# Kernel tuning notes

Hardware: AMD Instinct MI355X
Metric: run time of the kernel (lower is better)

Reference implementation:

```python
import jax, jax.numpy as jnp
import numpy as np

EPS = 1e-5
HEADS = 24
HEAD_DIM = 128


def _layernorm_noaffine(x):
    # LayerNorm over last dim (head_dim), elementwise_affine=False
    mu = jnp.mean(x, axis=-1, keepdims=True)
    var = jnp.mean(jnp.square(x - mu), axis=-1, keepdims=True)
    return (x - mu) / jnp.sqrt(var + EPS)


def _apply_rope(x, cos, sin):
    # diffusers apply_rotary_emb, use_real_unbind_dim=-2, sequence_dim=1
    # x: [B, S_img, H, D]; cos/sin: [S_img, D]
    x_real, x_imag = jnp.split(x, 2, axis=-1)               # halves of D
    x_rot = jnp.concatenate([-x_imag, x_real], axis=-1)
    return x * cos[None, :, None, :] + x_rot * sin[None, :, None, :]


def setup_inputs() -> dict:
    key = jax.random.key(0)
    ks = jax.random.split(key, 8)
    B, T, I, D = 2, 256, 1024, 3072
    inner = HEADS * HEAD_DIM
    return {
        "hidden_states": jax.random.normal(ks[0], (B, I, D), jnp.float32),
        "encoder_hidden_states": jax.random.normal(ks[1], (B, T, D), jnp.float32),
        "cos": jax.random.uniform(ks[2], (I, HEAD_DIM), jnp.float32),
        "sin": jax.random.uniform(ks[3], (I, HEAD_DIM), jnp.float32),
        "w_qkv": jax.random.normal(ks[4], (D, 3 * inner), jnp.float32) * 0.02,
        "b_qkv": jax.random.normal(ks[5], (3 * inner,), jnp.float32) * 0.02,
        "w_out": jax.random.normal(ks[6], (inner, D), jnp.float32) * 0.02,
        "b_out": jax.random.normal(ks[7], (D,), jnp.float32) * 0.02,
    }


def reference(hidden_states, encoder_hidden_states, cos, sin, w_qkv, b_qkv, w_out, b_out):
    text_len = encoder_hidden_states.shape[1]
    x = jnp.concatenate([encoder_hidden_states, hidden_states], axis=1)  # [B, S, D]
    B, S, _ = x.shape
    qkv = x @ w_qkv + b_qkv                                  # [B, S, 3*inner]
    q, k, v = jnp.split(qkv, 3, axis=-1)
    q = q.reshape(B, S, HEADS, HEAD_DIM)
    k = k.reshape(B, S, HEADS, HEAD_DIM)
    v = v.reshape(B, S, HEADS, HEAD_DIM)
    q = _layernorm_noaffine(q)
    k = _layernorm_noaffine(k)
    # partial RoPE: image tokens only
    q = jnp.concatenate([q[:, :text_len], _apply_rope(q[:, text_len:], cos, sin)], axis=1)
    k = jnp.concatenate([k[:, :text_len], _apply_rope(k[:, text_len:], cos, sin)], axis=1)
    # non-causal attention, scale = 1/sqrt(head_dim)
    scale = 1.0 / np.sqrt(HEAD_DIM).astype(np.float32)
    scores = jnp.einsum('bqhd,bkhd->bhqk', q, k) * scale
    attn = jax.nn.softmax(scores, axis=-1)
    out = jnp.einsum('bhqk,bkhd->bqhd', attn, v).reshape(B, S, HEADS * HEAD_DIM)
    out = out @ w_out + b_out                                # [B, S, D]
    return out[:, text_len:, :], out[:, :text_len, :]
```

## Files before the change

### kernel.cpp

```cpp
#include <hip/hip_runtime.h>

typedef unsigned short u16;
typedef __attribute__((ext_vector_type(8))) short bf16x8;
typedef __attribute__((ext_vector_type(4))) float f32x4;
typedef __attribute__((ext_vector_type(16))) float f32x16;

typedef const __attribute__((address_space(1))) void* gptr_t;
typedef __attribute__((address_space(3))) void* lptr_t;

__device__ __forceinline__ unsigned cvtpk_bf16(float a, float b){
  unsigned r; asm("v_cvt_pk_bf16_f32 %0, %1, %2" : "=v"(r) : "v"(a), "v"(b)); return r;
}
__device__ __forceinline__ u16 f2bf(float x){ return (u16)cvtpk_bf16(x, x); }
__device__ __forceinline__ float bf2f(u16 u){ union{unsigned i; float f;} v; v.i = ((unsigned)u)<<16; return v.f; }
__device__ __forceinline__ float fexp2(float x){ float r; asm("v_exp_f32 %0, %1" : "=v"(r) : "v"(x)); return r; }
__device__ __forceinline__ float vmax16(f32x16 v){
  float a0 = fmaxf(v[0],v[1]),  a1 = fmaxf(v[2],v[3]),  a2 = fmaxf(v[4],v[5]),  a3 = fmaxf(v[6],v[7]);
  float a4 = fmaxf(v[8],v[9]),  a5 = fmaxf(v[10],v[11]),a6 = fmaxf(v[12],v[13]),a7 = fmaxf(v[14],v[15]);
  float b0 = fmaxf(a0,a1), b1 = fmaxf(a2,a3), b2 = fmaxf(a4,a5), b3 = fmaxf(a6,a7);
  return fmaxf(fmaxf(b0,b1), fmaxf(b2,b3));
}

__global__ __launch_bounds__(256) void prep_x_kernel(const float* __restrict__ hs,
                                                     const float* __restrict__ ehs,
                                                     u16* __restrict__ A){
  int idx = blockIdx.x*256 + threadIdx.x;
  int v = idx*4;
  int m = v/3072, c = v - m*3072;
  int b = m/1280, s = m - b*1280;
  const float* src = (s < 256) ? (ehs + ((size_t)(b*256+s))*3072 + c)
                               : (hs  + ((size_t)(b*1024+(s-256)))*3072 + c);
  float4 f = *(const float4*)src;
  uint2 o; o.x = cvtpk_bf16(f.x, f.y); o.y = cvtpk_bf16(f.z, f.w);
  *(uint2*)(A + v) = o;
}

__global__ __launch_bounds__(256) void transpose_w_kernel(const float* __restrict__ W,
                                                          u16* __restrict__ Wt,
                                                          int K, int N){
  __shared__ float t[64][36];
  int k0 = blockIdx.y*64, n0 = blockIdx.x*32;
  int tid = threadIdx.x;
  #pragma unroll
  for (int i=0;i<2;i++){
    int cell = i*256 + tid; int kl = cell>>3, nc = cell&7;
    *(float4*)&t[kl][nc*4] = *(const float4*)&W[(size_t)(k0+kl)*N + n0 + nc*4];
  }
  __syncthreads();
  #pragma unroll
  for (int i=0;i<2;i++){
    int chunk = i*256 + tid; int nl = chunk>>4, kc = chunk&15;
    float a = t[kc*4+0][nl], b2 = t[kc*4+1][nl], c2 = t[kc*4+2][nl], d2 = t[kc*4+3][nl];
    uint2 u; u.x = cvtpk_bf16(a, b2); u.y = cvtpk_bf16(c2, d2);
    *(uint2*)&Wt[(size_t)(n0+nl)*K + k0 + kc*4] = u;
  }
}

__global__ __launch_bounds__(512) void gemm_qkv_kernel(const u16* __restrict__ A,
                                                       const u16* __restrict__ Bt,
                                                       const float* __restrict__ bias,
                                                       u16* __restrict__ C){
  const int K = 3072, N = 9216;
  __shared__ __align__(16) u16 lds[57344];
  int tid = threadIdx.x, wv = tid>>6, lane = tid&63;
  int wm = wv>>2, wn = wv&3;
  int l15 = lane&15, l4 = lane>>4;

  int bid = blockIdx.x;
  int wg = (bid&7)*60 + (bid>>3);
  int bm = wg/48, bn = wg%48;
  int m0 = bm*256, n0 = bn*192;

  int rlane = lane>>2;
  int schn = (lane&3) ^ ((lane>>3)&3);
  const u16* aS = A + (size_t)(m0 + wv*32 + rlane)*K + schn*8;
  int brow = n0 + wv*32 + rlane; if (brow > 9215) brow = 9215;
  const u16* bS = Bt + (size_t)brow*K + schn*8;

  auto stagePair = [&](int G){
    u16* base = lds + (G&3)*14336;
    size_t ko = (size_t)G*32;
    #pragma unroll
    for (int j=0;j<2;j++)
      __builtin_amdgcn_global_load_lds((gptr_t)(aS + (size_t)j*16*K + ko),
                                       (lptr_t)(base + (wv*2+j)*512), 16,0,0);
    if (wv < 6){
      #pragma unroll
      for (int j=0;j<2;j++)
        __builtin_amdgcn_global_load_lds((gptr_t)(bS + (size_t)j*16*K + ko),
                                         (lptr_t)(base + 8192 + (wv*2+j)*512), 16,0,0);
    }
  };

  int fcs = l4 ^ ((l15>>1)&3);
  f32x4 acc[8][3];
  #pragma unroll
  for (int r=0;r<8;r++)
    #pragma unroll
    for (int c=0;c<3;c++)
      #pragma unroll
      for (int q=0;q<4;q++) acc[r][c][q] = 0.f;

  stagePair(0); stagePair(1); stagePair(2);
  asm volatile("s_waitcnt vmcnt(4)" ::: "memory");
  __builtin_amdgcn_s_barrier();

  auto group = [&](int G, bool issue){
    const u16* rA = lds + (G&3)*14336;
    const u16* rB = rA + 8192;
    bf16x8 af[8], bfv[3];
    #pragma unroll
    for (int r=0;r<8;r++) af[r] = *(const bf16x8*)(rA + (wm*128 + r*16 + l15)*32 + fcs*8);
    #pragma unroll
    for (int c=0;c<3;c++) bfv[c] = *(const bf16x8*)(rB + (wn*48 + c*16 + l15)*32 + fcs*8);
    if (issue) stagePair(G+3);
    __builtin_amdgcn_s_setprio(1);
    #pragma unroll
    for (int r=0;r<8;r++)
      #pragma unroll
      for (int c=0;c<3;c++)
        acc[r][c] = __builtin_amdgcn_mfma_f32_16x16x32_bf16(af[r], bfv[c], acc[r][c], 0,0,0);
    __builtin_amdgcn_s_setprio(0);
  };

  for (int G=0; G<93; ++G){
    group(G, true);
    asm volatile("s_waitcnt vmcnt(4)" ::: "memory");
    __builtin_amdgcn_s_barrier();
  }
  group(93,false); asm volatile("s_waitcnt vmcnt(2)" ::: "memory"); __builtin_amdgcn_s_barrier();
  group(94,false); asm volatile("s_waitcnt vmcnt(0)" ::: "memory"); __builtin_amdgcn_s_barrier();
  group(95,false);

  #pragma unroll
  for (int r=0;r<8;r++){
    int row = m0 + wm*128 + r*16 + l4*4;
    #pragma unroll
    for (int c=0;c<3;c++){
      int col = n0 + wn*48 + c*16 + l15;
      float bv = bias[col];
      #pragma unroll
      for (int q=0;q<4;q++)
        C[(size_t)(row+q)*N + col] = f2bf(acc[r][c][q] + bv);
    }
  }
}

__global__ __launch_bounds__(256) void gemm_bt_kernel(const u16* __restrict__ A,
                                                      const u16* __restrict__ Bt,
                                                      const float* __restrict__ bias,
                                                      float* __restrict__ Cf,
                                                      int K, int N){
  __shared__ u16 As[2][4096];
  __shared__ u16 Bs[2][4096];
  int tid = threadIdx.x, wv = tid>>6, lane = tid&63;
  int l15 = lane & 15, l4 = lane >> 4;
  int m0 = blockIdx.y*128, n0 = blockIdx.x*128;
  int wr = wv>>1, wc = wv&1;

  f32x4 acc[4][4];
  #pragma unroll
  for (int i=0;i<4;i++)
    #pragma unroll
    for (int j=0;j<4;j++)
      #pragma unroll
      for (int r=0;r<4;r++) acc[i][j][r] = 0.f;

  const int NT = K >> 5;

  auto stage = [&](int buf, int kt){
    #pragma unroll
    for (int i=0;i<2;i++){
      int c = (wv*2+i)*64 + lane; int row = c>>2, kc = c&3;
      const u16* s = A + (size_t)(m0+row)*K + kt + kc*8;
      __builtin_amdgcn_global_load_lds((gptr_t)s, (lptr_t)(&As[buf][(wv*2+i)*512]), 16, 0, 0);
    }
    #pragma unroll
    for (int i=0;i<2;i++){
      int c = (wv*2+i)*64 + lane; int row = c>>2, kc = c&3;
      const u16* s = Bt + (size_t)(n0+row)*K + kt + kc*8;
      __builtin_amdgcn_global_load_lds((gptr_t)s, (lptr_t)(&Bs[buf][(wv*2+i)*512]), 16, 0, 0);
    }
  };

  stage(0, 0);
  __syncthreads();
  for (int t=0; t<NT; t++){
    int cur = t & 1;
    if (t+1 < NT) stage(cur^1, (t+1)*32);
    bf16x8 af[4], bfr[4];
    #pragma unroll
    for (int i=0;i<4;i++){
      af[i]  = *(const bf16x8*)&As[cur][(wr*64 + i*16 + l15)*32 + l4*8];
      bfr[i] = *(const bf16x8*)&Bs[cur][(wc*64 + i*16 + l15)*32 + l4*8];
    }
    #pragma unroll
    for (int i=0;i<4;i++)
      #pragma unroll
      for (int j=0;j<4;j++)
        acc[i][j] = __builtin_amdgcn_mfma_f32_16x16x32_bf16(af[i], bfr[j], acc[i][j], 0,0,0);
    __syncthreads();
  }

  #pragma unroll
  for (int i=0;i<4;i++){
    int row = m0 + wr*64 + i*16 + l4*4;
    #pragma unroll
    for (int j=0;j<4;j++){
      int col = n0 + wc*64 + j*16 + l15;
      float bv = bias[col];
      #pragma unroll
      for (int r=0;r<4;r++){
        int rr = row + r;
        int bb = rr / 1280; int s = rr - bb*1280;
        float* dst = (s < 256) ? (Cf + 6291456 + ((size_t)(bb*256 + s))*3072)
                               : (Cf + ((size_t)(bb*1024 + (s-256)))*3072);
        dst[col] = acc[i][j][r] + bv;
      }
    }
  }
}

__device__ __forceinline__ void ln_head(const u16* __restrict__ in, u16* __restrict__ out,
                                        const float* __restrict__ cosb, const float* __restrict__ sinb,
                                        int lane, int s, float scale){
  float x0 = bf2f(in[lane]), x1 = bf2f(in[64+lane]);
  float sum = x0 + x1;
  #pragma unroll
  for (int off=32; off>=1; off>>=1) sum += __shfl_xor(sum, off);
  float mean = sum * 0.0078125f;
  float d0 = x0-mean, d1 = x1-mean;
  float vs = d0*d0 + d1*d1;
  #pragma unroll
  for (int off=32; off>=1; off>>=1) vs += __shfl_xor(vs, off);
  float rstd = rsqrtf(vs*0.0078125f + 1e-5f);
  float y0 = d0*rstd, y1 = d1*rstd;
  if (s >= 256){
    int p = s - 256;
    float c0 = cosb[p*128 + lane], c1 = cosb[p*128 + 64 + lane];
    float s0 = sinb[p*128 + lane], s1 = sinb[p*128 + 64 + lane];
    float t0 = y0*c0 - y1*s0;
    float t1 = y1*c1 + y0*s1;
    y0 = t0; y1 = t1;
  }
  out[lane]    = f2bf(y0*scale);
  out[64+lane] = f2bf(y1*scale);
}

__global__ __launch_bounds__(256) void ln_rope_kernel(const u16* __restrict__ qkv,
                                                      const float* __restrict__ cosb,
                                                      const float* __restrict__ sinb,
                                                      u16* __restrict__ Q, u16* __restrict__ Kd){
  int g = blockIdx.x*4 + (threadIdx.x>>6);
  int lane = threadIdx.x & 63;
  int h = g % 24; int m = g / 24;
  int b = m / 1280; int s = m - b*1280;
  const u16* base = qkv + (size_t)m*9216 + h*128;
  size_t ho = ((size_t)(b*24 + h)*1280 + s)*128;
  ln_head(base,        Q  + ho, cosb, sinb, lane, s, 0.12751512f);
  ln_head(base + 3072, Kd + ho, cosb, sinb, lane, s, 1.0f);
}

__global__ __launch_bounds__(256) void v_transpose_kernel(const u16* __restrict__ qkv,
                                                          u16* __restrict__ Vt){
  __shared__ u16 tl[16384];
  int tid = threadIdx.x;
  int blk = blockIdx.x;
  int st = blk % 10; int bh = blk / 10; int b = bh/24, h = bh - b*24;
  #pragma unroll
  for (int i=0;i<8;i++){
    int idx = i*256 + tid; int s = idx>>4, dc = idx&15;
    int m = b*1280 + st*128 + s;
    bf16x8 v = *(const bf16x8*)(qkv + (size_t)m*9216 + 6144 + h*128 + dc*8);
    *(bf16x8*)(tl + (s*16 + (dc ^ ((s>>3)&7)))*8) = v;
  }
  __syncthreads();
  #pragma unroll
  for (int i=0;i<8;i++){
    int idx = i*256 + tid; int d = idx>>4, sc = idx&15;
    union { u16 t[8]; bf16x8 v; } tmp;
    #pragma unroll
    for (int j=0;j<8;j++){
      int s = sc*8 + j;
      tmp.t[j] = tl[(s*16 + ((d>>3) ^ ((s>>3)&7)))*8 + (d&7)];
    }
    *(bf16x8*)(Vt + ((size_t)bh*128 + d)*1280 + st*128 + sc*8) = tmp.v;
  }
}

__global__ __launch_bounds__(256) void attn_kernel(const u16* __restrict__ Q,
                                                   const u16* __restrict__ Kg,
                                                   const u16* __restrict__ Vt,
                                                   u16* __restrict__ AO){
  __shared__ __align__(16) u16 smem[32768];
  int tid = threadIdx.x, wv = tid>>6, lane = tid&63;
  int l31 = lane & 31, hi = lane >> 5;
  int blk = blockIdx.x;
  int qt = blk % 10; int bh = blk / 10;
  int b = bh / 24; int h = bh - b*24;
  const u16* Qb = Q  + (size_t)bh*1280*128;
  const u16* Kb = Kg + (size_t)bh*1280*128;
  const u16* Vb = Vt + (size_t)bh*128*1280;
  int q0 = qt*128 + wv*32;

  bf16x8 qf[8];
  #pragma unroll
  for (int ds=0; ds<8; ds++)
    qf[ds] = *(const bf16x8*)(Qb + (size_t)(q0 + l31)*128 + ds*16 + hi*8);

  f32x16 o[4];
  #pragma unroll
  for (int dc=0; dc<4; dc++)
    #pragma unroll
    for (int r=0;r<16;r++) o[dc][r] = 0.f;
  float mrun = -1e30f, lrun = 0.f;

  auto stage = [&](int t){
    int s0 = t*64; int bu = t&1;
    u16* Ksb = smem + bu*8192;
    u16* Vsb = smem + 16384 + bu*8192;
    #pragma unroll
    for (int i=0;i<4;i++){
      int c = (wv*4+i)*64 + lane; int key = c>>4, dc16 = c&15;
      const u16* src = Kb + (size_t)(s0+key)*128 + ((dc16 ^ (key&7))<<3);
      __builtin_amdgcn_global_load_lds((gptr_t)src, (lptr_t)(Ksb + (wv*4+i)*512), 16, 0, 0);
    }
    #pragma unroll
    for (int i=0;i<4;i++){
      int c = (wv*4+i)*64 + lane; int d = c>>3, kc = c&7;
      const u16* src = Vb + (size_t)d*1280 + s0 + ((kc ^ (d&7))<<3);
      __builtin_amdgcn_global_load_lds((gptr_t)src, (lptr_t)(Vsb + (wv*4+i)*512), 16, 0, 0);
    }
  };

  auto compute = [&](int t){
    const u16* Ks = smem + (t&1)*8192;
    const u16* Vs = smem + 16384 + (t&1)*8192;
    f32x16 sA, sB, sC, sD;
    #pragma unroll
    for (int r=0;r<16;r++){ sA[r]=0.f; sB[r]=0.f; sC[r]=0.f; sD[r]=0.f; }
    __builtin_amdgcn_s_setprio(1);
    #pragma unroll
    for (int dp=0; dp<4; dp++){
      int dsE = 2*dp, dsO = 2*dp+1;
      int chE = dsE*2 + hi, chO = dsO*2 + hi;
      bf16x8 k0E = *(const bf16x8*)(Ks + (l31*16      + (chE ^ (l31 & 7)))*8);
      bf16x8 k1E = *(const bf16x8*)(Ks + ((32+l31)*16 + (chE ^ (l31 & 7)))*8);
      bf16x8 k0O = *(const bf16x8*)(Ks + (l31*16      + (chO ^ (l31 & 7)))*8);
      bf16x8 k1O = *(const bf16x8*)(Ks + ((32+l31)*16 + (chO ^ (l31 & 7)))*8);
      sA = __builtin_amdgcn_mfma_f32_32x32x16_bf16(k0E, qf[dsE], sA, 0,0,0);
      sC = __builtin_amdgcn_mfma_f32_32x32x16_bf16(k1E, qf[dsE], sC, 0,0,0);
      sB = __builtin_amdgcn_mfma_f32_32x32x16_bf16(k0O, qf[dsO], sB, 0,0,0);
      sD = __builtin_amdgcn_mfma_f32_32x32x16_bf16(k1O, qf[dsO], sD, 0,0,0);
    }
    __builtin_amdgcn_s_setprio(0);
    f32x16 sacc0, sacc1;
    #pragma unroll
    for (int r=0;r<16;r++){ sacc0[r] = sA[r]+sB[r]; sacc1[r] = sC[r]+sD[r]; }

    float mt = fmaxf(vmax16(sacc0), vmax16(sacc1));
    mt = fmaxf(mt, __shfl_xor(mt, 32));
    int noresc = __all(mt <= mrun + 11.5f);
    float mnew, corr;
    if (noresc){ mnew = mrun; corr = 1.f; }
    else       { mnew = fmaxf(mrun, mt); corr = fexp2(mrun - mnew); }
    mrun = mnew;
    float p[32];
    float ps0=0.f, ps1=0.f, ps2=0.f, ps3=0.f;
    #pragma unroll
    for (int r=0;r<8;r++){ p[r]    = fexp2(sacc0[r]   - mnew); ps0 += p[r]; }
    #pragma unroll
    for (int r=0;r<8;r++){ p[8+r]  = fexp2(sacc0[8+r] - mnew); ps1 += p[8+r]; }
    #pragma unroll
    for (int r=0;r<8;r++){ p[16+r] = fexp2(sacc1[r]   - mnew); ps2 += p[16+r]; }
    #pragma unroll
    for (int r=0;r<8;r++){ p[24+r] = fexp2(sacc1[8+r] - mnew); ps3 += p[24+r]; }
    float ps = (ps0+ps1) + (ps2+ps3);
    ps += __shfl_xor(ps, 32);
    lrun = lrun*corr + ps;
    if (!noresc){
      #pragma unroll
      for (int dc=0; dc<4; dc++)
        #pragma unroll
        for (int r=0;r<16;r++) o[dc][r] *= corr;
    }

    bf16x8 pf[4];
    #pragma unroll
    for (int c=0;c<4;c++){
      const float* pp = p + (c>>1)*16 + (c&1)*8;
      unsigned x0 = cvtpk_bf16(pp[0], pp[1]);
      unsigned y0 = cvtpk_bf16(pp[4], pp[5]);
      unsigned x1 = cvtpk_bf16(pp[2], pp[3]);
      unsigned y1 = cvtpk_bf16(pp[6], pp[7]);
      asm volatile("v_permlane32_swap_b32 %0, %1" : "+v"(x0), "+v"(y0));
      asm volatile("v_permlane32_swap_b32 %0, %1" : "+v"(x1), "+v"(y1));
      union { unsigned u[4]; bf16x8 v; } wb;
      wb.u[0]=x0; wb.u[1]=x1; wb.u[2]=y0; wb.u[3]=y1;
      pf[c] = wb.v;
    }
    __builtin_amdgcn_s_setprio(1);
    #pragma unroll
    for (int c=0;c<4;c++){
      #pragma unroll
      for (int dc=0;dc<4;dc++){
        int d = dc*32 + l31;
        bf16x8 vf = *(const bf16x8*)(Vs + (d*8 + ((2*c+hi) ^ (d&7)))*8);
        o[dc] = __builtin_amdgcn_mfma_f32_32x32x16_bf16(vf, pf[c], o[dc], 0,0,0);
      }
    }
    __builtin_amdgcn_s_setprio(0);
  };

  stage(0); stage(1);
  for (int t=0; t<19; ++t){
    asm volatile("s_waitcnt vmcnt(8)" ::: "memory");
    __builtin_amdgcn_s_barrier();
    compute(t);
    __builtin_amdgcn_s_barrier();
    if (t <= 17) stage(t+2);
  }
  asm volatile("s_waitcnt vmcnt(0)" ::: "memory");
  __builtin_amdgcn_s_barrier();
  compute(19);

  float rl = 1.f / lrun;
  __syncthreads();
  u16* ob = smem + wv*4096;
  #pragma unroll
  for (int dc=0; dc<4; dc++){
    #pragma unroll
    for (int rp=0; rp<8; rp++){
      int d = dc*32 + 2*(rp&1) + 8*(rp>>1) + 4*hi;
      unsigned u = cvtpk_bf16(o[dc][2*rp]*rl, o[dc][2*rp+1]*rl);
      int chs = (d>>3) ^ (l31 & 7);
      *(unsigned*)(ob + l31*128 + chs*8 + (d&7)) = u;
    }
  }
  __syncthreads();
  #pragma unroll
  for (int i=0;i<8;i++){
    int idx = i*64 + lane; int q = idx>>4, c8 = idx&15;
    bf16x8 vv = *(const bf16x8*)(ob + q*128 + ((c8 ^ (q&7))<<3));
    *(bf16x8*)(AO + (size_t)(b*1280 + q0 + q)*3072 + h*128 + c8*8) = vv;
  }
}

extern "C" void kernel_launch(void* const* d_in, const int* in_sizes, int n_in,
                              void* d_out, int out_size, void* d_ws, size_t ws_size,
                              hipStream_t stream){
  (void)in_sizes; (void)n_in; (void)out_size; (void)ws_size;
  const float* hs   = (const float*)d_in[0];
  const float* ehs  = (const float*)d_in[1];
  const float* cosb = (const float*)d_in[2];
  const float* sinb = (const float*)d_in[3];
  const float* wqkv = (const float*)d_in[4];
  const float* bqkv = (const float*)d_in[5];
  const float* wout = (const float*)d_in[6];
  const float* bout = (const float*)d_in[7];
  char* w = (char*)d_ws;
  size_t o = 0;
  u16* Abf = (u16*)(w + o); o += 15728640ull;
  u16* WqT = (u16*)(w + o); o += 56623104ull;
  u16* WoT = (u16*)(w + o); o += 18874368ull;
  u16* qkv = (u16*)(w + o); o += 47185920ull;
  u16* Qd  = (u16*)(w + o); o += 15728640ull;
  u16* Kd  = (u16*)(w + o); o += 15728640ull;
  u16* Vtd = (u16*)(w + o); o += 15728640ull;
  u16* AO  = (u16*)(w + o);
  float* out = (float*)d_out;

  prep_x_kernel<<<7680, 256, 0, stream>>>(hs, ehs, Abf);
  transpose_w_kernel<<<dim3(288,48), 256, 0, stream>>>(wqkv, WqT, 3072, 9216);
  transpose_w_kernel<<<dim3(96,48),  256, 0, stream>>>(wout, WoT, 3072, 3072);
  gemm_qkv_kernel<<<480, 512, 0, stream>>>(Abf, WqT, bqkv, qkv);
  ln_rope_kernel<<<15360, 256, 0, stream>>>(qkv, cosb, sinb, Qd, Kd);
  v_transpose_kernel<<<480, 256, 0, stream>>>(qkv, Vtd);
  attn_kernel<<<480, 256, 0, stream>>>(Qd, Kd, Vtd, AO);
  gemm_bt_kernel<<<dim3(24,20), 256, 0, stream>>>(AO, WoT, bout, out, 3072, 3072);
}
```

Before: 558.2 us.

## Enlarge attention and output GEMM tiles to 512 threads with XCD-aware block remap

The output projection GEMM moves from 128x128 tiles with 256 threads and double buffering to 256x128 tiles with 512 threads, a 4-deep LDS ring, swizzled LDS layout and s_waitcnt-based pipelining, mirroring the QKV GEMM. The attention kernel now processes 256 queries per block with 8 waves sharing each staged K/V tile, which halves global K/V traffic per query. Both kernels remap block IDs so that consecutive tiles land on the same XCD. The cost is fewer blocks (240) on a 256-CU device, which may leave some CUs idle, plus higher LDS and register pressure.

```diff
diff --git a/kernel.cpp b/kernel.cpp
--- a/kernel.cpp
+++ b/kernel.cpp
@@ -146,76 +146,91 @@
   }
 }
 
-__global__ __launch_bounds__(256) void gemm_bt_kernel(const u16* __restrict__ A,
-                                                      const u16* __restrict__ Bt,
-                                                      const float* __restrict__ bias,
-                                                      float* __restrict__ Cf,
-                                                      int K, int N){
-  __shared__ u16 As[2][4096];
-  __shared__ u16 Bs[2][4096];
+__global__ __launch_bounds__(512) void gemm_out_kernel(const u16* __restrict__ A,
+                                                       const u16* __restrict__ Bt,
+                                                       const float* __restrict__ bias,
+                                                       float* __restrict__ Cf){
+  const int K = 3072;
+  __shared__ __align__(16) u16 lds[49152];
   int tid = threadIdx.x, wv = tid>>6, lane = tid&63;
-  int l15 = lane & 15, l4 = lane >> 4;
-  int m0 = blockIdx.y*128, n0 = blockIdx.x*128;
-  int wr = wv>>1, wc = wv&1;
-
-  f32x4 acc[4][4];
-  #pragma unroll
-  for (int i=0;i<4;i++)
-    #pragma unroll
-    for (int j=0;j<4;j++)
-      #pragma unroll
-      for (int r=0;r<4;r++) acc[i][j][r] = 0.f;
-
-  const int NT = K >> 5;
-
-  auto stage = [&](int buf, int kt){
-    #pragma unroll
-    for (int i=0;i<2;i++){
-      int c = (wv*2+i)*64 + lane; int row = c>>2, kc = c&3;
-      const u16* s = A + (size_t)(m0+row)*K + kt + kc*8;
-      __builtin_amdgcn_global_load_lds((gptr_t)s, (lptr_t)(&As[buf][(wv*2+i)*512]), 16, 0, 0);
-    }
-    #pragma unroll
-    for (int i=0;i<2;i++){
-      int c = (wv*2+i)*64 + lane; int row = c>>2, kc = c&3;
-      const u16* s = Bt + (size_t)(n0+row)*K + kt + kc*8;
-      __builtin_amdgcn_global_load_lds((gptr_t)s, (lptr_t)(&Bs[buf][(wv*2+i)*512]), 16, 0, 0);
-    }
-  };
-
-  stage(0, 0);
-  __syncthreads();
-  for (int t=0; t<NT; t++){
-    int cur = t & 1;
-    if (t+1 < NT) stage(cur^1, (t+1)*32);
-    bf16x8 af[4], bfr[4];
-    #pragma unroll
-    for (int i=0;i<4;i++){
-      af[i]  = *(const bf16x8*)&As[cur][(wr*64 + i*16 + l15)*32 + l4*8];
-      bfr[i] = *(const bf16x8*)&Bs[cur][(wc*64 + i*16 + l15)*32 + l4*8];
-    }
-    #pragma unroll
-    for (int i=0;i<4;i++)
-      #pragma unroll
-      for (int j=0;j<4;j++)
-        acc[i][j] = __builtin_amdgcn_mfma_f32_16x16x32_bf16(af[i], bfr[j], acc[i][j], 0,0,0);
-    __syncthreads();
-  }
-
-  #pragma unroll
-  for (int i=0;i<4;i++){
-    int row = m0 + wr*64 + i*16 + l4*4;
-    #pragma unroll
-    for (int j=0;j<4;j++){
-      int col = n0 + wc*64 + j*16 + l15;
+  int wm = wv>>2, wn = wv&3;
+  int l15 = lane&15, l4 = lane>>4;
+
+  int bid = blockIdx.x;
+  int wg = (bid&7)*30 + (bid>>3);
+  int bm = wg/24, bn = wg%24;
+  int m0 = bm*256, n0 = bn*128;
+
+  int rlane = lane>>2;
+  int schn = (lane&3) ^ ((lane>>3)&3);
+  const u16* aS = A  + (size_t)(m0 + wv*32 + rlane)*K + schn*8;
+  const u16* bS = Bt + (size_t)(n0 + (tid>>2))*K + schn*8;
+
+  auto stagePair = [&](int G){
+    u16* base = lds + (G&3)*12288;
+    size_t ko = (size_t)G*32;
+    #pragma unroll
+    for (int j=0;j<2;j++)
+      __builtin_amdgcn_global_load_lds((gptr_t)(aS + (size_t)j*16*K + ko),
+                                       (lptr_t)(base + (wv*2+j)*512), 16,0,0);
+    __builtin_amdgcn_global_load_lds((gptr_t)(bS + ko),
+                                     (lptr_t)(base + 8192 + wv*512), 16,0,0);
+  };
+
+  int fcs = l4 ^ ((l15>>1)&3);
+  f32x4 acc[8][2];
+  #pragma unroll
+  for (int r=0;r<8;r++)
+    #pragma unroll
+    for (int c=0;c<2;c++)
+      #pragma unroll
+      for (int q=0;q<4;q++) acc[r][c][q] = 0.f;
+
+  stagePair(0); stagePair(1); stagePair(2);
+  asm volatile("s_waitcnt vmcnt(6)" ::: "memory");
+  __builtin_amdgcn_s_barrier();
+
+  auto group = [&](int G, bool issue){
+    const u16* rA = lds + (G&3)*12288;
+    const u16* rB = rA + 8192;
+    bf16x8 af[8], bfv[2];
+    #pragma unroll
+    for (int r=0;r<8;r++) af[r] = *(const bf16x8*)(rA + (wm*128 + r*16 + l15)*32 + fcs*8);
+    #pragma unroll
+    for (int c=0;c<2;c++) bfv[c] = *(const bf16x8*)(rB + (wn*32 + c*16 + l15)*32 + fcs*8);
+    if (issue) stagePair(G+3);
+    __builtin_amdgcn_s_setprio(1);
+    #pragma unroll
+    for (int r=0;r<8;r++)
+      #pragma unroll
+      for (int c=0;c<2;c++)
+        acc[r][c] = __builtin_amdgcn_mfma_f32_16x16x32_bf16(af[r], bfv[c], acc[r][c], 0,0,0);
+    __builtin_amdgcn_s_setprio(0);
+  };
+
+  for (int G=0; G<93; ++G){
+    group(G, true);
+    asm volatile("s_waitcnt vmcnt(6)" ::: "memory");
+    __builtin_amdgcn_s_barrier();
+  }
+  group(93,false); asm volatile("s_waitcnt vmcnt(3)" ::: "memory"); __builtin_amdgcn_s_barrier();
+  group(94,false); asm volatile("s_waitcnt vmcnt(0)" ::: "memory"); __builtin_amdgcn_s_barrier();
+  group(95,false);
+
+  #pragma unroll
+  for (int r=0;r<8;r++){
+    int row = m0 + wm*128 + r*16 + l4*4;
+    #pragma unroll
+    for (int c=0;c<2;c++){
+      int col = n0 + wn*32 + c*16 + l15;
       float bv = bias[col];
       #pragma unroll
-      for (int r=0;r<4;r++){
-        int rr = row + r;
+      for (int q=0;q<4;q++){
+        int rr = row + q;
         int bb = rr / 1280; int s = rr - bb*1280;
         float* dst = (s < 256) ? (Cf + 6291456 + ((size_t)(bb*256 + s))*3072)
                                : (Cf + ((size_t)(bb*1024 + (s-256)))*3072);
-        dst[col] = acc[i][j][r] + bv;
+        dst[col] = acc[r][c][q] + bv;
       }
     }
   }
@@ -288,20 +303,21 @@
   }
 }
 
-__global__ __launch_bounds__(256) void attn_kernel(const u16* __restrict__ Q,
+__global__ __launch_bounds__(512) void attn_kernel(const u16* __restrict__ Q,
                                                    const u16* __restrict__ Kg,
                                                    const u16* __restrict__ Vt,
                                                    u16* __restrict__ AO){
   __shared__ __align__(16) u16 smem[32768];
   int tid = threadIdx.x, wv = tid>>6, lane = tid&63;
   int l31 = lane & 31, hi = lane >> 5;
-  int blk = blockIdx.x;
-  int qt = blk % 10; int bh = blk / 10;
+  int bid = blockIdx.x;
+  int wg = (bid&7)*30 + (bid>>3);
+  int qt = wg % 5; int bh = wg / 5;
   int b = bh / 24; int h = bh - b*24;
   const u16* Qb = Q  + (size_t)bh*1280*128;
   const u16* Kb = Kg + (size_t)bh*1280*128;
   const u16* Vb = Vt + (size_t)bh*128*1280;
-  int q0 = qt*128 + wv*32;
+  int q0 = qt*256 + wv*32;
 
   bf16x8 qf[8];
   #pragma unroll
@@ -320,16 +336,16 @@
     u16* Ksb = smem + bu*8192;
     u16* Vsb = smem + 16384 + bu*8192;
     #pragma unroll
-    for (int i=0;i<4;i++){
-      int c = (wv*4+i)*64 + lane; int key = c>>4, dc16 = c&15;
+    for (int i=0;i<2;i++){
+      int c = i*512 + tid; int key = c>>4, dc16 = c&15;
       const u16* src = Kb + (size_t)(s0+key)*128 + ((dc16 ^ (key&7))<<3);
-      __builtin_amdgcn_global_load_lds((gptr_t)src, (lptr_t)(Ksb + (wv*4+i)*512), 16, 0, 0);
-    }
-    #pragma unroll
-    for (int i=0;i<4;i++){
-      int c = (wv*4+i)*64 + lane; int d = c>>3, kc = c&7;
+      __builtin_amdgcn_global_load_lds((gptr_t)src, (lptr_t)(Ksb + i*4096 + wv*512), 16, 0, 0);
+    }
+    #pragma unroll
+    for (int i=0;i<2;i++){
+      int c = i*512 + tid; int d = c>>3, kc = c&7;
       const u16* src = Vb + (size_t)d*1280 + s0 + ((kc ^ (d&7))<<3);
-      __builtin_amdgcn_global_load_lds((gptr_t)src, (lptr_t)(Vsb + (wv*4+i)*512), 16, 0, 0);
+      __builtin_amdgcn_global_load_lds((gptr_t)src, (lptr_t)(Vsb + i*4096 + wv*512), 16, 0, 0);
     }
   };
 
@@ -414,7 +430,7 @@
 
   stage(0); stage(1);
   for (int t=0; t<19; ++t){
-    asm volatile("s_waitcnt vmcnt(8)" ::: "memory");
+    asm volatile("s_waitcnt vmcnt(4)" ::: "memory");
     __builtin_amdgcn_s_barrier();
     compute(t);
     __builtin_amdgcn_s_barrier();
@@ -476,6 +492,6 @@
   gemm_qkv_kernel<<<480, 512, 0, stream>>>(Abf, WqT, bqkv, qkv);
   ln_rope_kernel<<<15360, 256, 0, stream>>>(qkv, cosb, sinb, Qd, Kd);
   v_transpose_kernel<<<480, 256, 0, stream>>>(qkv, Vtd);
-  attn_kernel<<<480, 256, 0, stream>>>(Qd, Kd, Vtd, AO);
-  gemm_bt_kernel<<<dim3(24,20), 256, 0, stream>>>(AO, WoT, bout, out, 3072, 3072);
-}
+  attn_kernel<<<240, 512, 0, stream>>>(Qd, Kd, Vtd, AO);
+  gemm_out_kernel<<<240, 512, 0, stream>>>(AO, WoT, bout, out);
+}
```

Measured after the change: 519.4 us. 6.9% less time.
